# Kernel tuning notes

Measured on AMD Instinct MI355X. Metric: run time of the kernel, lower is better.

The kernel has to match this reference:

```python
import jax, jax.numpy as jnp
import numpy as np

DIM = 1024
HEADS = 8
DIM_HEAD = 64
INNER = HEADS * DIM_HEAD
NQ = 4096
NKV = 4096
SCALE = DIM_HEAD ** (-0.5)
NEG = -1.0e9


def setup_inputs() -> dict:
    key = jax.random.key(0)
    ks = jax.random.split(key, 7)
    s = DIM ** (-0.5)
    x = jax.random.normal(ks[0], (NQ, DIM), dtype=jnp.float32)
    y = jax.random.normal(ks[1], (NKV, DIM), dtype=jnp.float32)
    # binary mask: 1 => blocked (gets -1e9 added), 0 => attend
    mask = jax.random.randint(ks[2], (NQ, NKV), 0, 2).astype(jnp.float32)
    Wq = jax.random.normal(ks[3], (DIM, INNER), dtype=jnp.float32) * s
    Wk = jax.random.normal(ks[4], (DIM, INNER), dtype=jnp.float32) * s
    Wv = jax.random.normal(ks[5], (DIM, INNER), dtype=jnp.float32) * s
    Wo = jax.random.normal(ks[6], (INNER, DIM), dtype=jnp.float32) * (INNER ** -0.5)
    return {"x": x, "y": y, "mask": mask, "Wq": Wq, "Wk": Wk, "Wv": Wv, "Wo": Wo}


def reference(x, y, mask, Wq, Wk, Wv, Wo):
    # q scaled before projection split, as in the torch module
    q = (x @ Wq) * SCALE                      # [NQ, INNER]
    k = y @ Wk                                # [NKV, INNER]
    v = y @ Wv                                # [NKV, INNER]
    qh = q.reshape(NQ, HEADS, DIM_HEAD)
    kh = k.reshape(NKV, HEADS, DIM_HEAD)
    vh = v.reshape(NKV, HEADS, DIM_HEAD)
    # per-head QK^T + additive mask (mask shared across heads), then softmax
    scores = jnp.einsum('nhd,mhd->hnm', qh, kh) + mask * NEG  # [H, NQ, NKV]
    attn = jax.nn.softmax(scores, axis=-1)
    outh = jnp.einsum('hnm,mhd->nhd', attn, vh)               # [NQ, H, D]
    out = outh.reshape(NQ, INNER) @ Wo                        # [NQ, DIM]
    return out
```

## Files before the change

### kernel.cpp

```cpp
#include <hip/hip_runtime.h>

#define DIMM   1024
#define INNER  512
#define HEADS  8
#define DH     64
#define NQ     4096
#define NKV    4096
#define NSPLIT 4
#define KVCHUNK (NKV / NSPLIT)
#define QBLK   32
#define MWORDS (NKV / 32)
#define LOG2E  (1.44269504089f)
#define SM_C   (-17.3123404907f)

typedef __attribute__((ext_vector_type(8))) short s16x8;
typedef __attribute__((ext_vector_type(4))) short s16x4;
typedef __attribute__((ext_vector_type(4))) float f32x4;
typedef __attribute__((ext_vector_type(4))) unsigned int u32x4;
typedef short s16x2a __attribute__((ext_vector_type(2), may_alias));
typedef s16x8 s16x8a __attribute__((may_alias));

__device__ __forceinline__ short f2b(float x) {
    unsigned int u = __float_as_uint(x);
    unsigned int r = (u + 0x7fffu + ((u >> 16) & 1u)) >> 16;
    return (short)r;
}

__device__ __forceinline__ float fast_exp2(float x) {
#if __has_builtin(__builtin_amdgcn_exp2f)
    return __builtin_amdgcn_exp2f(x);
#else
    return exp2f(x);
#endif
}

__global__ __launch_bounds__(256) void conv_xy(const float* __restrict__ x,
                                               const float* __restrict__ y,
                                               short* __restrict__ xb,
                                               short* __restrict__ yb) {
    const size_t NX = (size_t)NQ * DIMM;
    size_t i = ((size_t)blockIdx.x * 256 + threadIdx.x) * 4;
    const float* s; short* d; size_t o;
    if (i < NX) { s = x; d = xb; o = i; } else { s = y; d = yb; o = i - NX; }
    f32x4 v = *(const f32x4*)(s + o);
    s16x4 b;
#pragma unroll
    for (int j = 0; j < 4; ++j) b[j] = f2b(v[j]);
    *(s16x4*)(d + o) = b;
}

__global__ __launch_bounds__(256) void conv_w(const float* __restrict__ Wq,
                                              const float* __restrict__ Wk,
                                              const float* __restrict__ Wv,
                                              const float* __restrict__ Wo,
                                              short* __restrict__ Wcat,
                                              short* __restrict__ Wot) {
    int idx = blockIdx.x * 256 + threadIdx.x;
    int which = idx >> 19;
    int e = idx & 524287;
    if (which == 3) { int k = e >> 10, n = e & 1023; Wot[(size_t)n * INNER + k] = f2b(Wo[e]); }
    else {
        const float* W = (which == 0) ? Wq : (which == 1) ? Wk : Wv;
        float sc = (which == 0) ? 0.125f : 1.0f;
        int k = e >> 9, n = e & 511;
        Wcat[(size_t)(which * 512 + n) * DIMM + k] = f2b(W[e] * sc);
    }
}

__global__ __launch_bounds__(256) void conv_mask(const float* __restrict__ mask,
                                                 unsigned int* __restrict__ Mb) {
    int wg = blockIdx.x * 4 + (threadIdx.x >> 6);
    int l = threadIdx.x & 63;
    for (int itr = 0; itr < 32; ++itr) {
        size_t i = (size_t)wg * 32 + itr;
        int q = (int)(i >> 6), c = (int)(i & 63);
        float v = mask[(size_t)q * NKV + c * 64 + l];
        unsigned long long b = __ballot(v != 0.0f);
        if ((l & 31) == 0) Mb[(size_t)q * MWORDS + c * 2 + (l >> 5)] = (unsigned int)(b >> l);
    }
}

__global__ __launch_bounds__(256) void gemm_qkv(const short* __restrict__ xb,
                                                const short* __restrict__ yb,
                                                const short* __restrict__ Wcat,
                                                short* __restrict__ Qb,
                                                short* __restrict__ Kb,
                                                short* __restrict__ Vt) {
    __shared__ __align__(16) short Ash[128 * 40];
    __shared__ __align__(16) short Bsh[128 * 40];
    const int t = threadIdx.x, w = t >> 6, l = t & 63, l15 = l & 15, q4 = l >> 4;
    const int m0 = blockIdx.x * 128;
    const int by = blockIdx.y;
    const int n0 = by * 128;
    const short* A = (by < 4) ? xb : yb;
    const int wm = (w >> 1) * 64, wn = (w & 1) * 64;
    f32x4 acc[4][4] = {};

    for (int ks = 0; ks < DIMM; ks += 32) {
        __syncthreads();
#pragma unroll
        for (int j = 0; j < 2; ++j) {
            int c = t + j * 256;
            int row = c >> 2, cb = c & 3;
            s16x8 va = *(const s16x8*)&A   [(size_t)(m0 + row) * DIMM + ks + cb * 8];
            s16x8 vb = *(const s16x8*)&Wcat[(size_t)(n0 + row) * DIMM + ks + cb * 8];
            *(s16x8*)&Ash[row * 40 + cb * 8] = va;
            *(s16x8*)&Bsh[row * 40 + cb * 8] = vb;
        }
        __syncthreads();
        s16x8 af[4], bf[4];
#pragma unroll
        for (int i = 0; i < 4; ++i) af[i] = *(const s16x8*)&Ash[(wm + i * 16 + l15) * 40 + q4 * 8];
#pragma unroll
        for (int i = 0; i < 4; ++i) bf[i] = *(const s16x8*)&Bsh[(wn + i * 16 + l15) * 40 + q4 * 8];
#pragma unroll
        for (int mi = 0; mi < 4; ++mi)
#pragma unroll
            for (int ni = 0; ni < 4; ++ni)
                acc[mi][ni] = __builtin_amdgcn_mfma_f32_16x16x32_bf16(af[mi], bf[ni], acc[mi][ni], 0, 0, 0);
    }

#pragma unroll
    for (int mi = 0; mi < 4; ++mi)
#pragma unroll
        for (int ni = 0; ni < 4; ++ni)
#pragma unroll
            for (int r = 0; r < 4; ++r) {
                int row = m0 + wm + mi * 16 + q4 * 4 + r;
                int n = n0 + wn + ni * 16 + l15;
                short b = f2b(acc[mi][ni][r]);
                if (n < 512)       Qb[(size_t)row * INNER + n] = b;
                else if (n < 1024) Kb[(size_t)row * INNER + (n - 512)] = b;
                else               Vt[(size_t)(n - 1024) * NKV + row] = b;
            }
}

__global__ __launch_bounds__(256, 4) void attn_fused(const short* __restrict__ Qb,
                                                     const short* __restrict__ Kb,
                                                     const short* __restrict__ Vt,
                                                     const unsigned int* __restrict__ Mb,
                                                     float* __restrict__ Op,
                                                     float* __restrict__ lpart) {
    __shared__ __align__(16) unsigned int Msh[32 * 32];
    __shared__ __align__(16) short Psh[4 * 32 * 40];
    const int t = threadIdx.x, w = t >> 6, l = t & 63, l15 = l & 15, q4 = l >> 4;
    const int q0 = blockIdx.x * QBLK;
    const int split = blockIdx.y;
    const int h = blockIdx.z * 4 + w;
    const int kv_base = split * KVCHUNK;
    short* Pw = Psh + w * (32 * 40);

    {
        int it = t & 31, r8 = t >> 5;
#pragma unroll
        for (int jj = 0; jj < 4; ++jj) {
            int row = r8 + jj * 8;
            Msh[it * 32 + row] = Mb[(size_t)(q0 + row) * MWORDS + split * 32 + it];
        }
    }

    s16x8 qf[2][2];
#pragma unroll
    for (int mi = 0; mi < 2; ++mi)
#pragma unroll
        for (int kb = 0; kb < 2; ++kb)
            qf[mi][kb] = *(const s16x8*)&Qb[(size_t)(q0 + mi * 16 + l15) * INNER + h * DH + kb * 32 + q4 * 8];

    __syncthreads();

    f32x4 accO[2][4] = {};
    float lsum[2][4] = {};

    for (int it = 0; it < KVCHUNK / 32; ++it) {
        const int kv0 = kv_base + it * 32;
        s16x8 kf[2][2];
#pragma unroll
        for (int ni = 0; ni < 2; ++ni)
#pragma unroll
            for (int kb = 0; kb < 2; ++kb)
                kf[ni][kb] = *(const s16x8*)&Kb[(size_t)(kv0 + 2 * l15 + ni) * INNER + h * DH + kb * 32 + q4 * 8];
        s16x8 vf[4];
#pragma unroll
        for (int ni = 0; ni < 4; ++ni)
            vf[ni] = *(const s16x8*)&Vt[(size_t)(h * DH + ni * 16 + l15) * NKV + kv0 + q4 * 8];

        f32x4 sf[2][2] = {};
#pragma unroll
        for (int mi = 0; mi < 2; ++mi)
#pragma unroll
            for (int ni = 0; ni < 2; ++ni) {
                sf[mi][ni] = __builtin_amdgcn_mfma_f32_16x16x32_bf16(qf[mi][0], kf[ni][0], sf[mi][ni], 0, 0, 0);
                sf[mi][ni] = __builtin_amdgcn_mfma_f32_16x16x32_bf16(qf[mi][1], kf[ni][1], sf[mi][ni], 0, 0, 0);
            }

#pragma unroll
        for (int mi = 0; mi < 2; ++mi) {
            u32x4 w4 = *(const u32x4*)&Msh[it * 32 + mi * 16 + q4 * 4];
#pragma unroll
            for (int r = 0; r < 4; ++r) {
                unsigned int sh = w4[r] >> (2 * l15);
                float e0 = fast_exp2(fmaf(sf[mi][0][r], LOG2E, SM_C));
                float e1 = fast_exp2(fmaf(sf[mi][1][r], LOG2E, SM_C));
                float p0 = (sh & 1u) ? 0.0f : e0;
                float p1 = (sh & 2u) ? 0.0f : e1;
                lsum[mi][r] += p0 + p1;
                unsigned int pk;
                asm("v_cvt_pk_bf16_f32 %0, %1, %2" : "=v"(pk) : "v"(p0), "v"(p1));
                *(s16x2a*)&Pw[(mi * 16 + q4 * 4 + r) * 40 + 2 * l15] = __builtin_bit_cast(s16x2a, pk);
            }
        }

        s16x8 pf[2];
#pragma unroll
        for (int mi = 0; mi < 2; ++mi)
            pf[mi] = (s16x8)(*(const s16x8a*)&Pw[(mi * 16 + l15) * 40 + q4 * 8]);
#pragma unroll
        for (int mi = 0; mi < 2; ++mi)
#pragma unroll
            for (int ni = 0; ni < 4; ++ni)
                accO[mi][ni] = __builtin_amdgcn_mfma_f32_16x16x32_bf16(pf[mi], vf[ni], accO[mi][ni], 0, 0, 0);
    }

#pragma unroll
    for (int mi = 0; mi < 2; ++mi)
#pragma unroll
        for (int ni = 0; ni < 4; ++ni)
#pragma unroll
            for (int r = 0; r < 4; ++r) {
                int q = q0 + mi * 16 + q4 * 4 + r;
                Op[((size_t)split * NQ + q) * INNER + h * DH + ni * 16 + l15] = accO[mi][ni][r];
            }
#pragma unroll
    for (int mi = 0; mi < 2; ++mi)
#pragma unroll
        for (int r = 0; r < 4; ++r) {
            float s = lsum[mi][r];
            s += __shfl_xor(s, 1);
            s += __shfl_xor(s, 2);
            s += __shfl_xor(s, 4);
            s += __shfl_xor(s, 8);
            lsum[mi][r] = s;
        }
    if (l15 == 0) {
#pragma unroll
        for (int mi = 0; mi < 2; ++mi)
#pragma unroll
            for (int r = 0; r < 4; ++r) {
                int q = q0 + mi * 16 + q4 * 4 + r;
                lpart[((size_t)split * NQ + q) * HEADS + h] = lsum[mi][r];
            }
    }
}

__global__ __launch_bounds__(256) void merge_kernel(const float* __restrict__ Op,
                                                    const float* __restrict__ lpart,
                                                    short* __restrict__ AO) {
    int idx = blockIdx.x * 256 + threadIdx.x;
    int q = idx >> 6, dc = idx & 63, h = dc >> 3;
    float L = 0.f;
#pragma unroll
    for (int s = 0; s < NSPLIT; ++s) L += lpart[((size_t)s * NQ + q) * HEADS + h];
    f32x4 a0 = {}, a1 = {};
#pragma unroll
    for (int s = 0; s < NSPLIT; ++s) {
        const f32x4* p = (const f32x4*)&Op[((size_t)s * NQ + q) * INNER + dc * 8];
        a0 += p[0];
        a1 += p[1];
    }
    float inv = 1.0f / L;
    s16x8 o;
#pragma unroll
    for (int j = 0; j < 4; ++j) o[j] = f2b(a0[j] * inv);
#pragma unroll
    for (int j = 0; j < 4; ++j) o[4 + j] = f2b(a1[j] * inv);
    *(s16x8*)&AO[(size_t)q * INNER + dc * 8] = o;
}

__global__ __launch_bounds__(256) void gemm_out(const short* __restrict__ A,
                                                const short* __restrict__ Bt,
                                                float* __restrict__ C) {
    __shared__ __align__(16) short Ash[128 * 40];
    __shared__ __align__(16) short Bsh[128 * 40];
    const int t = threadIdx.x, w = t >> 6, l = t & 63, l15 = l & 15, q4 = l >> 4;
    const int m0 = blockIdx.x * 128, n0 = blockIdx.y * 128;
    const int wm = (w >> 1) * 64, wn = (w & 1) * 64;
    f32x4 acc[4][4] = {};

    for (int ks = 0; ks < INNER; ks += 32) {
        __syncthreads();
#pragma unroll
        for (int j = 0; j < 2; ++j) {
            int c = t + j * 256;
            int row = c >> 2, cb = c & 3;
            s16x8 va = *(const s16x8*)&A [(size_t)(m0 + row) * INNER + ks + cb * 8];
            s16x8 vb = *(const s16x8*)&Bt[(size_t)(n0 + row) * INNER + ks + cb * 8];
            *(s16x8*)&Ash[row * 40 + cb * 8] = va;
            *(s16x8*)&Bsh[row * 40 + cb * 8] = vb;
        }
        __syncthreads();
        s16x8 af[4], bf[4];
#pragma unroll
        for (int i = 0; i < 4; ++i) af[i] = *(const s16x8*)&Ash[(wm + i * 16 + l15) * 40 + q4 * 8];
#pragma unroll
        for (int i = 0; i < 4; ++i) bf[i] = *(const s16x8*)&Bsh[(wn + i * 16 + l15) * 40 + q4 * 8];
#pragma unroll
        for (int mi = 0; mi < 4; ++mi)
#pragma unroll
            for (int ni = 0; ni < 4; ++ni)
                acc[mi][ni] = __builtin_amdgcn_mfma_f32_16x16x32_bf16(af[mi], bf[ni], acc[mi][ni], 0, 0, 0);
    }

#pragma unroll
    for (int mi = 0; mi < 4; ++mi)
#pragma unroll
        for (int ni = 0; ni < 4; ++ni)
#pragma unroll
            for (int r = 0; r < 4; ++r) {
                int row = m0 + wm + mi * 16 + q4 * 4 + r;
                int col = n0 + wn + ni * 16 + l15;
                C[(size_t)row * DIMM + col] = acc[mi][ni][r];
            }
}

extern "C" void kernel_launch(void* const* d_in, const int* in_sizes, int n_in,
                              void* d_out, int out_size, void* d_ws, size_t ws_size,
                              hipStream_t stream) {
    const float* x    = (const float*)d_in[0];
    const float* y    = (const float*)d_in[1];
    const float* mask = (const float*)d_in[2];
    const float* Wq   = (const float*)d_in[3];
    const float* Wk   = (const float*)d_in[4];
    const float* Wv   = (const float*)d_in[5];
    const float* Wo   = (const float*)d_in[6];
    float* out = (float*)d_out;

    char* ws = (char*)d_ws;
    float* Op    = (float*)(ws + (size_t)0);
    short* xb    = (short*)(ws + (size_t)0);
    short* yb    = (short*)(ws + ((size_t)8  << 20));
    short* Qb    = (short*)(ws + ((size_t)32 << 20));
    short* Kb    = (short*)(ws + ((size_t)36 << 20));
    short* Vtb   = (short*)(ws + ((size_t)40 << 20));
    short* AO    = (short*)(ws + ((size_t)44 << 20));
    unsigned int* Mb = (unsigned int*)(ws + ((size_t)48 << 20));
    float* lpart = (float*)(ws + ((size_t)50 << 20));
    short* Wcat  = (short*)(ws + ((size_t)51 << 20));
    short* Wot   = (short*)(ws + ((size_t)54 << 20));

    hipLaunchKernelGGL(conv_xy,   dim3(8192), dim3(256), 0, stream, x, y, xb, yb);
    hipLaunchKernelGGL(conv_w,    dim3(8192), dim3(256), 0, stream, Wq, Wk, Wv, Wo, Wcat, Wot);
    hipLaunchKernelGGL(conv_mask, dim3(2048), dim3(256), 0, stream, mask, Mb);
    hipLaunchKernelGGL(gemm_qkv,  dim3(32, 12), dim3(256), 0, stream, xb, yb, Wcat, Qb, Kb, Vtb);
    hipLaunchKernelGGL(attn_fused, dim3(128, NSPLIT, 2), dim3(256), 0, stream,
                       Qb, Kb, Vtb, Mb, Op, lpart);
    hipLaunchKernelGGL(merge_kernel, dim3(1024), dim3(256), 0, stream, Op, lpart, AO);
    hipLaunchKernelGGL(gemm_out,  dim3(32, 8), dim3(256), 0, stream, AO, Wot, out);
}
```

Measured before the change: 337.2 us.

## Fuse x/y bf16 conversion into QKV GEMM and halve M tiles

Drops the separate conv_xy kernel and converts fp32 x/y to bf16 while staging A tiles inside gemm_qkv. This removes one launch and a full bf16 write and reread of the activations. Both GEMMs shrink their M tile from 128 to 64 rows, and attention shrinks its query block from 32 to 16 rows with a higher occupancy bound. These give more workgroups on the MI355X at the cost of less reuse per tile, so K/V fragments and weight tiles are reloaded more often.

```diff
diff --git a/kernel.cpp b/kernel.cpp
--- a/kernel.cpp
+++ b/kernel.cpp
@@ -8,7 +8,7 @@
 #define NKV    4096
 #define NSPLIT 4
 #define KVCHUNK (NKV / NSPLIT)
-#define QBLK   32
+#define QBLK   16
 #define MWORDS (NKV / 32)
 #define LOG2E  (1.44269504089f)
 #define SM_C   (-17.3123404907f)
@@ -32,21 +32,6 @@
 #else
     return exp2f(x);
 #endif
-}
-
-__global__ __launch_bounds__(256) void conv_xy(const float* __restrict__ x,
-                                               const float* __restrict__ y,
-                                               short* __restrict__ xb,
-                                               short* __restrict__ yb) {
-    const size_t NX = (size_t)NQ * DIMM;
-    size_t i = ((size_t)blockIdx.x * 256 + threadIdx.x) * 4;
-    const float* s; short* d; size_t o;
-    if (i < NX) { s = x; d = xb; o = i; } else { s = y; d = yb; o = i - NX; }
-    f32x4 v = *(const f32x4*)(s + o);
-    s16x4 b;
-#pragma unroll
-    for (int j = 0; j < 4; ++j) b[j] = f2b(v[j]);
-    *(s16x4*)(d + o) = b;
 }
 
 __global__ __launch_bounds__(256) void conv_w(const float* __restrict__ Wq,
@@ -80,48 +65,56 @@
     }
 }
 
-__global__ __launch_bounds__(256) void gemm_qkv(const short* __restrict__ xb,
-                                                const short* __restrict__ yb,
+__global__ __launch_bounds__(256) void gemm_qkv(const float* __restrict__ x,
+                                                const float* __restrict__ y,
                                                 const short* __restrict__ Wcat,
                                                 short* __restrict__ Qb,
                                                 short* __restrict__ Kb,
                                                 short* __restrict__ Vt) {
-    __shared__ __align__(16) short Ash[128 * 40];
+    __shared__ __align__(16) short Ash[64 * 40];
     __shared__ __align__(16) short Bsh[128 * 40];
     const int t = threadIdx.x, w = t >> 6, l = t & 63, l15 = l & 15, q4 = l >> 4;
-    const int m0 = blockIdx.x * 128;
+    const int m0 = blockIdx.x * 64;
     const int by = blockIdx.y;
     const int n0 = by * 128;
-    const short* A = (by < 4) ? xb : yb;
-    const int wm = (w >> 1) * 64, wn = (w & 1) * 64;
-    f32x4 acc[4][4] = {};
+    const float* A = (by < 4) ? x : y;
+    const int wm = (w >> 1) * 32, wn = (w & 1) * 64;
+    f32x4 acc[2][4] = {};
+
+    const int arow = t >> 2, aseg = t & 3;
 
     for (int ks = 0; ks < DIMM; ks += 32) {
         __syncthreads();
+        {
+            const f32x4* pa = (const f32x4*)&A[(size_t)(m0 + arow) * DIMM + ks + aseg * 8];
+            f32x4 a0 = pa[0], a1 = pa[1];
+            s16x8 ab;
+#pragma unroll
+            for (int j = 0; j < 4; ++j) { ab[j] = f2b(a0[j]); ab[4 + j] = f2b(a1[j]); }
+            *(s16x8*)&Ash[arow * 40 + aseg * 8] = ab;
+        }
 #pragma unroll
         for (int j = 0; j < 2; ++j) {
             int c = t + j * 256;
-            int row = c >> 2, cb = c & 3;
-            s16x8 va = *(const s16x8*)&A   [(size_t)(m0 + row) * DIMM + ks + cb * 8];
-            s16x8 vb = *(const s16x8*)&Wcat[(size_t)(n0 + row) * DIMM + ks + cb * 8];
-            *(s16x8*)&Ash[row * 40 + cb * 8] = va;
-            *(s16x8*)&Bsh[row * 40 + cb * 8] = vb;
+            int row = c >> 2, seg = c & 3;
+            s16x8 vb = *(const s16x8*)&Wcat[(size_t)(n0 + row) * DIMM + ks + seg * 8];
+            *(s16x8*)&Bsh[row * 40 + seg * 8] = vb;
         }
         __syncthreads();
-        s16x8 af[4], bf[4];
-#pragma unroll
-        for (int i = 0; i < 4; ++i) af[i] = *(const s16x8*)&Ash[(wm + i * 16 + l15) * 40 + q4 * 8];
+        s16x8 af[2], bf[4];
+#pragma unroll
+        for (int i = 0; i < 2; ++i) af[i] = *(const s16x8*)&Ash[(wm + i * 16 + l15) * 40 + q4 * 8];
 #pragma unroll
         for (int i = 0; i < 4; ++i) bf[i] = *(const s16x8*)&Bsh[(wn + i * 16 + l15) * 40 + q4 * 8];
 #pragma unroll
-        for (int mi = 0; mi < 4; ++mi)
+        for (int mi = 0; mi < 2; ++mi)
 #pragma unroll
             for (int ni = 0; ni < 4; ++ni)
                 acc[mi][ni] = __builtin_amdgcn_mfma_f32_16x16x32_bf16(af[mi], bf[ni], acc[mi][ni], 0, 0, 0);
     }
 
 #pragma unroll
-    for (int mi = 0; mi < 4; ++mi)
+    for (int mi = 0; mi < 2; ++mi)
 #pragma unroll
         for (int ni = 0; ni < 4; ++ni)
 #pragma unroll
@@ -135,41 +128,39 @@
             }
 }
 
-__global__ __launch_bounds__(256, 4) void attn_fused(const short* __restrict__ Qb,
+__global__ __launch_bounds__(256, 8) void attn_fused(const short* __restrict__ Qb,
                                                      const short* __restrict__ Kb,
                                                      const short* __restrict__ Vt,
                                                      const unsigned int* __restrict__ Mb,
                                                      float* __restrict__ Op,
                                                      float* __restrict__ lpart) {
-    __shared__ __align__(16) unsigned int Msh[32 * 32];
-    __shared__ __align__(16) short Psh[4 * 32 * 40];
+    __shared__ __align__(16) unsigned int Msh[32 * QBLK];
+    __shared__ __align__(16) short Psh[4 * QBLK * 40];
     const int t = threadIdx.x, w = t >> 6, l = t & 63, l15 = l & 15, q4 = l >> 4;
     const int q0 = blockIdx.x * QBLK;
     const int split = blockIdx.y;
     const int h = blockIdx.z * 4 + w;
     const int kv_base = split * KVCHUNK;
-    short* Pw = Psh + w * (32 * 40);
+    short* Pw = Psh + w * (QBLK * 40);
 
     {
         int it = t & 31, r8 = t >> 5;
 #pragma unroll
-        for (int jj = 0; jj < 4; ++jj) {
+        for (int jj = 0; jj < 2; ++jj) {
             int row = r8 + jj * 8;
-            Msh[it * 32 + row] = Mb[(size_t)(q0 + row) * MWORDS + split * 32 + it];
-        }
-    }
-
-    s16x8 qf[2][2];
-#pragma unroll
-    for (int mi = 0; mi < 2; ++mi)
-#pragma unroll
-        for (int kb = 0; kb < 2; ++kb)
-            qf[mi][kb] = *(const s16x8*)&Qb[(size_t)(q0 + mi * 16 + l15) * INNER + h * DH + kb * 32 + q4 * 8];
+            Msh[it * QBLK + row] = Mb[(size_t)(q0 + row) * MWORDS + split * 32 + it];
+        }
+    }
+
+    s16x8 qf[2];
+#pragma unroll
+    for (int kb = 0; kb < 2; ++kb)
+        qf[kb] = *(const s16x8*)&Qb[(size_t)(q0 + l15) * INNER + h * DH + kb * 32 + q4 * 8];
 
     __syncthreads();
 
-    f32x4 accO[2][4] = {};
-    float lsum[2][4] = {};
+    f32x4 accO[4] = {};
+    float lsum[4] = {};
 
     for (int it = 0; it < KVCHUNK / 32; ++it) {
         const int kv0 = kv_base + it * 32;
@@ -184,71 +175,57 @@
         for (int ni = 0; ni < 4; ++ni)
             vf[ni] = *(const s16x8*)&Vt[(size_t)(h * DH + ni * 16 + l15) * NKV + kv0 + q4 * 8];
 
-        f32x4 sf[2][2] = {};
-#pragma unroll
-        for (int mi = 0; mi < 2; ++mi)
-#pragma unroll
-            for (int ni = 0; ni < 2; ++ni) {
-                sf[mi][ni] = __builtin_amdgcn_mfma_f32_16x16x32_bf16(qf[mi][0], kf[ni][0], sf[mi][ni], 0, 0, 0);
-                sf[mi][ni] = __builtin_amdgcn_mfma_f32_16x16x32_bf16(qf[mi][1], kf[ni][1], sf[mi][ni], 0, 0, 0);
-            }
-
-#pragma unroll
-        for (int mi = 0; mi < 2; ++mi) {
-            u32x4 w4 = *(const u32x4*)&Msh[it * 32 + mi * 16 + q4 * 4];
+        f32x4 sf[2] = {};
+#pragma unroll
+        for (int ni = 0; ni < 2; ++ni) {
+            sf[ni] = __builtin_amdgcn_mfma_f32_16x16x32_bf16(qf[0], kf[ni][0], sf[ni], 0, 0, 0);
+            sf[ni] = __builtin_amdgcn_mfma_f32_16x16x32_bf16(qf[1], kf[ni][1], sf[ni], 0, 0, 0);
+        }
+
+        {
+            u32x4 w4 = *(const u32x4*)&Msh[it * QBLK + q4 * 4];
 #pragma unroll
             for (int r = 0; r < 4; ++r) {
                 unsigned int sh = w4[r] >> (2 * l15);
-                float e0 = fast_exp2(fmaf(sf[mi][0][r], LOG2E, SM_C));
-                float e1 = fast_exp2(fmaf(sf[mi][1][r], LOG2E, SM_C));
+                float e0 = fast_exp2(fmaf(sf[0][r], LOG2E, SM_C));
+                float e1 = fast_exp2(fmaf(sf[1][r], LOG2E, SM_C));
                 float p0 = (sh & 1u) ? 0.0f : e0;
                 float p1 = (sh & 2u) ? 0.0f : e1;
-                lsum[mi][r] += p0 + p1;
+                lsum[r] += p0 + p1;
                 unsigned int pk;
                 asm("v_cvt_pk_bf16_f32 %0, %1, %2" : "=v"(pk) : "v"(p0), "v"(p1));
-                *(s16x2a*)&Pw[(mi * 16 + q4 * 4 + r) * 40 + 2 * l15] = __builtin_bit_cast(s16x2a, pk);
+                *(s16x2a*)&Pw[(q4 * 4 + r) * 40 + 2 * l15] = __builtin_bit_cast(s16x2a, pk);
             }
         }
 
-        s16x8 pf[2];
-#pragma unroll
-        for (int mi = 0; mi < 2; ++mi)
-            pf[mi] = (s16x8)(*(const s16x8a*)&Pw[(mi * 16 + l15) * 40 + q4 * 8]);
-#pragma unroll
-        for (int mi = 0; mi < 2; ++mi)
-#pragma unroll
-            for (int ni = 0; ni < 4; ++ni)
-                accO[mi][ni] = __builtin_amdgcn_mfma_f32_16x16x32_bf16(pf[mi], vf[ni], accO[mi][ni], 0, 0, 0);
-    }
-
-#pragma unroll
-    for (int mi = 0; mi < 2; ++mi)
+        s16x8 pf = (s16x8)(*(const s16x8a*)&Pw[l15 * 40 + q4 * 8]);
 #pragma unroll
         for (int ni = 0; ni < 4; ++ni)
-#pragma unroll
-            for (int r = 0; r < 4; ++r) {
-                int q = q0 + mi * 16 + q4 * 4 + r;
-                Op[((size_t)split * NQ + q) * INNER + h * DH + ni * 16 + l15] = accO[mi][ni][r];
-            }
-#pragma unroll
-    for (int mi = 0; mi < 2; ++mi)
+            accO[ni] = __builtin_amdgcn_mfma_f32_16x16x32_bf16(pf, vf[ni], accO[ni], 0, 0, 0);
+    }
+
+#pragma unroll
+    for (int ni = 0; ni < 4; ++ni)
 #pragma unroll
         for (int r = 0; r < 4; ++r) {
-            float s = lsum[mi][r];
-            s += __shfl_xor(s, 1);
-            s += __shfl_xor(s, 2);
-            s += __shfl_xor(s, 4);
-            s += __shfl_xor(s, 8);
-            lsum[mi][r] = s;
-        }
+            int q = q0 + q4 * 4 + r;
+            Op[((size_t)split * NQ + q) * INNER + h * DH + ni * 16 + l15] = accO[ni][r];
+        }
+#pragma unroll
+    for (int r = 0; r < 4; ++r) {
+        float s = lsum[r];
+        s += __shfl_xor(s, 1);
+        s += __shfl_xor(s, 2);
+        s += __shfl_xor(s, 4);
+        s += __shfl_xor(s, 8);
+        lsum[r] = s;
+    }
     if (l15 == 0) {
 #pragma unroll
-        for (int mi = 0; mi < 2; ++mi)
-#pragma unroll
-            for (int r = 0; r < 4; ++r) {
-                int q = q0 + mi * 16 + q4 * 4 + r;
-                lpart[((size_t)split * NQ + q) * HEADS + h] = lsum[mi][r];
-            }
+        for (int r = 0; r < 4; ++r) {
+            int q = q0 + q4 * 4 + r;
+            lpart[((size_t)split * NQ + q) * HEADS + h] = lsum[r];
+        }
     }
 }
 
@@ -279,39 +256,42 @@
 __global__ __launch_bounds__(256) void gemm_out(const short* __restrict__ A,
                                                 const short* __restrict__ Bt,
                                                 float* __restrict__ C) {
-    __shared__ __align__(16) short Ash[128 * 40];
+    __shared__ __align__(16) short Ash[64 * 40];
     __shared__ __align__(16) short Bsh[128 * 40];
     const int t = threadIdx.x, w = t >> 6, l = t & 63, l15 = l & 15, q4 = l >> 4;
-    const int m0 = blockIdx.x * 128, n0 = blockIdx.y * 128;
-    const int wm = (w >> 1) * 64, wn = (w & 1) * 64;
-    f32x4 acc[4][4] = {};
+    const int m0 = blockIdx.x * 64, n0 = blockIdx.y * 128;
+    const int wm = (w >> 1) * 32, wn = (w & 1) * 64;
+    f32x4 acc[2][4] = {};
+    const int arow = t >> 2, aseg = t & 3;
 
     for (int ks = 0; ks < INNER; ks += 32) {
         __syncthreads();
+        {
+            s16x8 va = *(const s16x8*)&A[(size_t)(m0 + arow) * INNER + ks + aseg * 8];
+            *(s16x8*)&Ash[arow * 40 + aseg * 8] = va;
+        }
 #pragma unroll
         for (int j = 0; j < 2; ++j) {
             int c = t + j * 256;
-            int row = c >> 2, cb = c & 3;
-            s16x8 va = *(const s16x8*)&A [(size_t)(m0 + row) * INNER + ks + cb * 8];
-            s16x8 vb = *(const s16x8*)&Bt[(size_t)(n0 + row) * INNER + ks + cb * 8];
-            *(s16x8*)&Ash[row * 40 + cb * 8] = va;
-            *(s16x8*)&Bsh[row * 40 + cb * 8] = vb;
+            int row = c >> 2, seg = c & 3;
+            s16x8 vb = *(const s16x8*)&Bt[(size_t)(n0 + row) * INNER + ks + seg * 8];
+            *(s16x8*)&Bsh[row * 40 + seg * 8] = vb;
         }
         __syncthreads();
-        s16x8 af[4], bf[4];
-#pragma unroll
-        for (int i = 0; i < 4; ++i) af[i] = *(const s16x8*)&Ash[(wm + i * 16 + l15) * 40 + q4 * 8];
+        s16x8 af[2], bf[4];
+#pragma unroll
+        for (int i = 0; i < 2; ++i) af[i] = *(const s16x8*)&Ash[(wm + i * 16 + l15) * 40 + q4 * 8];
 #pragma unroll
         for (int i = 0; i < 4; ++i) bf[i] = *(const s16x8*)&Bsh[(wn + i * 16 + l15) * 40 + q4 * 8];
 #pragma unroll
-        for (int mi = 0; mi < 4; ++mi)
+        for (int mi = 0; mi < 2; ++mi)
 #pragma unroll
             for (int ni = 0; ni < 4; ++ni)
                 acc[mi][ni] = __builtin_amdgcn_mfma_f32_16x16x32_bf16(af[mi], bf[ni], acc[mi][ni], 0, 0, 0);
     }
 
 #pragma unroll
-    for (int mi = 0; mi < 4; ++mi)
+    for (int mi = 0; mi < 2; ++mi)
 #pragma unroll
         for (int ni = 0; ni < 4; ++ni)
 #pragma unroll
@@ -336,8 +316,6 @@
 
     char* ws = (char*)d_ws;
     float* Op    = (float*)(ws + (size_t)0);
-    short* xb    = (short*)(ws + (size_t)0);
-    short* yb    = (short*)(ws + ((size_t)8  << 20));
     short* Qb    = (short*)(ws + ((size_t)32 << 20));
     short* Kb    = (short*)(ws + ((size_t)36 << 20));
     short* Vtb   = (short*)(ws + ((size_t)40 << 20));
@@ -347,12 +325,11 @@
     short* Wcat  = (short*)(ws + ((size_t)51 << 20));
     short* Wot   = (short*)(ws + ((size_t)54 << 20));
 
-    hipLaunchKernelGGL(conv_xy,   dim3(8192), dim3(256), 0, stream, x, y, xb, yb);
     hipLaunchKernelGGL(conv_w,    dim3(8192), dim3(256), 0, stream, Wq, Wk, Wv, Wo, Wcat, Wot);
     hipLaunchKernelGGL(conv_mask, dim3(2048), dim3(256), 0, stream, mask, Mb);
-    hipLaunchKernelGGL(gemm_qkv,  dim3(32, 12), dim3(256), 0, stream, xb, yb, Wcat, Qb, Kb, Vtb);
-    hipLaunchKernelGGL(attn_fused, dim3(128, NSPLIT, 2), dim3(256), 0, stream,
+    hipLaunchKernelGGL(gemm_qkv,  dim3(64, 12), dim3(256), 0, stream, x, y, Wcat, Qb, Kb, Vtb);
+    hipLaunchKernelGGL(attn_fused, dim3(NQ / QBLK, NSPLIT, 2), dim3(256), 0, stream,
                        Qb, Kb, Vtb, Mb, Op, lpart);
     hipLaunchKernelGGL(merge_kernel, dim3(1024), dim3(256), 0, stream, Op, lpart, AO);
-    hipLaunchKernelGGL(gemm_out,  dim3(32, 8), dim3(256), 0, stream, AO, Wot, out);
-}
+    hipLaunchKernelGGL(gemm_out,  dim3(64, 8), dim3(256), 0, stream, AO, Wot, out);
+}
```

Measured after the change: 448.9 us. 1.33x slower.
